# Performance work log

Measured on AMD Instinct MI355X. Metric: run time of the kernel, lower is better.

## Reference

```python
import jax, jax.numpy as jnp
import numpy as np

N_POINTS = 1048576
LEVELS = 16
LOG2T = 19
TABLE_SIZE = 1 << LOG2T  # 524288
FEAT = 2
MIN_RES = 16.0
MAX_RES = 512.0


def setup_inputs() -> dict:
    key = jax.random.key(0)
    kx, kt = jax.random.split(key)
    bounding_box = jnp.array([[-1.5, -1.5, -1.5], [1.5, 1.5, 1.5]], dtype=jnp.float32)
    # sample mostly inside the box, a few points slightly outside to exercise clamp/keep_mask
    x = jax.random.uniform(kx, (N_POINTS, 3), dtype=jnp.float32, minval=-1.6, maxval=1.6)
    # torch init: uniform(-1e-4, 1e-4) per level embedding table
    tables = jax.random.uniform(kt, (LEVELS, TABLE_SIZE, FEAT), dtype=jnp.float32,
                                minval=-1e-4, maxval=1e-4)
    return {"x": x, "bounding_box": bounding_box, "tables": tables}


def _hash_encode(x, bounding_box, tables):
    min_b, max_b = bounding_box[0], bounding_box[1]  # [3]
    # keep_mask: point unchanged by clamping in every dim
    keep_mask = jnp.all((x >= min_b) & (x <= max_b), axis=-1)
    xc = jnp.clip(x, min_b, max_b)
    u = (xc - min_b) / (max_b - min_b)  # normalized to [0,1], [N,3]

    b = jnp.exp((jnp.log(MAX_RES) - jnp.log(MIN_RES)) / (LEVELS - 1))
    PI = jnp.array([1, 2654435761, 805459861], dtype=jnp.uint32)
    HASH_MASK = jnp.uint32(TABLE_SIZE - 1)
    # 8 corner offsets in (i,j,k) order matching the torch module
    offs = jnp.array([[i, j, k] for i in (0, 1) for j in (0, 1) for k in (0, 1)],
                     dtype=jnp.int32)  # [8,3]

    outs = []
    for level in range(LEVELS):
        Nl = jnp.floor(MIN_RES * b ** level)            # scalar resolution
        box_size = (max_b - min_b) / Nl                 # [3]
        grid = jnp.floor(u * Nl).astype(jnp.int32)      # [N,3] min-corner grid coords
        vmin = grid.astype(x.dtype) * box_size + min_b  # [N,3]
        vmax = vmin + box_size                          # [N,3]
        corners = (grid[:, None, :] + offs[None, :, :]).astype(jnp.uint32)  # [N,8,3]
        # spatial hash: xor of coord*prime, wrap-around in uint32 matches low bits of torch int64
        h = (corners[..., 0] * PI[0]) ^ (corners[..., 1] * PI[1]) ^ (corners[..., 2] * PI[2])
        idx = (h & HASH_MASK).astype(jnp.int32)         # [N,8]
        emb = tables[level][idx]                        # gather -> [N,8,F]
        # trilinear interpolation; note: uses ORIGINAL (unclamped) x, as in the torch code
        w = (x - vmin) / (vmax - vmin)                  # [N,3]
        wx, wy, wz = w[:, 0:1], w[:, 1:2], w[:, 2:3]
        c00 = emb[:, 0] * (1 - wx) + emb[:, 4] * wx
        c01 = emb[:, 1] * (1 - wx) + emb[:, 5] * wx
        c10 = emb[:, 2] * (1 - wx) + emb[:, 6] * wx
        c11 = emb[:, 3] * (1 - wx) + emb[:, 7] * wx
        c0 = c00 * (1 - wy) + c10 * wy
        c1 = c01 * (1 - wy) + c11 * wy
        outs.append(c0 * (1 - wz) + c1 * wz)            # [N,F]
    return jnp.concatenate(outs, axis=-1), keep_mask    # [N, L*F], [N]


def reference(x, bounding_box, tables):
    return _hash_encode(x, bounding_box, tables)
```

## Files before the change

### kernel.cpp

```cpp
#include <hip/hip_runtime.h>

#define NPTS   1048576
#define NLEV   16
#define TSIZE  (1u << 19)
#define HMASK  (TSIZE - 1u)
#define NBUCK  32768

__device__ __constant__ float NLF_TAB[16] = {
    16.f, 20.f, 25.f, 32.f, 40.f, 50.f, 64.f, 80.f,
    101.f, 128.f, 161.f, 203.f, 256.f, 322.f, 406.f, 512.f};

__device__ __forceinline__ unsigned spread5(unsigned x) {
    x &= 0x1F;
    x = (x | (x << 8)) & 0x100F;
    x = (x | (x << 4)) & 0x10C3;
    x = (x | (x << 2)) & 0x1249;
    return x;
}

__device__ __forceinline__ unsigned morton_key(float u0, float u1, float u2) {
    unsigned k0 = min(31u, (unsigned)(u0 * 32.0f));
    unsigned k1 = min(31u, (unsigned)(u1 * 32.0f));
    unsigned k2 = min(31u, (unsigned)(u2 * 32.0f));
    return (spread5(k0) << 2) | (spread5(k1) << 1) | spread5(k2);
}

__device__ __forceinline__ void uvw(float x0, float x1, float x2,
                                    float* u0, float* u1, float* u2) {
    const float mn = -1.5f, mx = 1.5f, rng = 3.0f;
    *u0 = (fminf(fmaxf(x0, mn), mx) - mn) / rng;
    *u1 = (fminf(fmaxf(x1, mn), mx) - mn) / rng;
    *u2 = (fminf(fmaxf(x2, mn), mx) - mn) / rng;
}

__device__ __forceinline__ void level_lerp(
    float x0, float x1, float x2, float u0, float u1, float u2,
    float Nl, const float2* __restrict__ tab, float* r0, float* r1)
{
#pragma clang fp contract(off)
    const float mn = -1.5f, rng = 3.0f;
    const float box = rng / Nl;

    int g0 = (int)floorf(u0 * Nl);
    int g1 = (int)floorf(u1 * Nl);
    int g2 = (int)floorf(u2 * Nl);

    float vmin0 = (float)g0 * box + mn;
    float vmin1 = (float)g1 * box + mn;
    float vmin2 = (float)g2 * box + mn;

    float den0 = (vmin0 + box) - vmin0;
    float den1 = (vmin1 + box) - vmin1;
    float den2 = (vmin2 + box) - vmin2;

    float wx = (x0 - vmin0) / den0;
    float wy = (x1 - vmin1) / den1;
    float wz = (x2 - vmin2) / den2;

    unsigned hx0 = (unsigned)g0;
    unsigned hx1 = (unsigned)(g0 + 1);
    unsigned hy0 = (unsigned)g1       * 2654435761u;
    unsigned hy1 = (unsigned)(g1 + 1) * 2654435761u;
    unsigned hz0 = (unsigned)g2       * 805459861u;
    unsigned hz1 = (unsigned)(g2 + 1) * 805459861u;

    float2 e000 = tab[(hx0 ^ hy0 ^ hz0) & HMASK];
    float2 e001 = tab[(hx0 ^ hy0 ^ hz1) & HMASK];
    float2 e010 = tab[(hx0 ^ hy1 ^ hz0) & HMASK];
    float2 e011 = tab[(hx0 ^ hy1 ^ hz1) & HMASK];
    float2 e100 = tab[(hx1 ^ hy0 ^ hz0) & HMASK];
    float2 e101 = tab[(hx1 ^ hy0 ^ hz1) & HMASK];
    float2 e110 = tab[(hx1 ^ hy1 ^ hz0) & HMASK];
    float2 e111 = tab[(hx1 ^ hy1 ^ hz1) & HMASK];

    float omx = 1.0f - wx, omy = 1.0f - wy, omz = 1.0f - wz;
    {
        float c00 = e000.x * omx + e100.x * wx;
        float c01 = e001.x * omx + e101.x * wx;
        float c10 = e010.x * omx + e110.x * wx;
        float c11 = e011.x * omx + e111.x * wx;
        float c0  = c00 * omy + c10 * wy;
        float c1  = c01 * omy + c11 * wy;
        *r0 = c0 * omz + c1 * wz;
    }
    {
        float c00 = e000.y * omx + e100.y * wx;
        float c01 = e001.y * omx + e101.y * wx;
        float c10 = e010.y * omx + e110.y * wx;
        float c11 = e011.y * omx + e111.y * wx;
        float c0  = c00 * omy + c10 * wy;
        float c1  = c01 * omy + c11 * wy;
        *r1 = c0 * omz + c1 * wz;
    }
}


template<int L, bool DO_HIST, bool DO_MASK>
__device__ __forceinline__ void fine_body(
    const float* __restrict__ xin, const float* __restrict__ tables,
    float* __restrict__ out, unsigned* __restrict__ hist, int p)
{
#pragma clang fp contract(off)
    float x0 = xin[3 * p], x1 = xin[3 * p + 1], x2 = xin[3 * p + 2];
    float u0, u1, u2; uvw(x0, x1, x2, &u0, &u1, &u2);

    if (DO_HIST)
        atomicAdd(&hist[morton_key(u0, u1, u2)], 1u);

    const float2* tab = (const float2*)tables + (size_t)L * TSIZE;
    float r0, r1;
    level_lerp(x0, x1, x2, u0, u1, u2, NLF_TAB[L], tab, &r0, &r1);
    *(float2*)(out + (size_t)p * 32 + 2 * L) = make_float2(r0, r1);

    if (DO_MASK) {
        const float mn = -1.5f, mx = 1.5f;
        float keep = (x0 >= mn && x0 <= mx &&
                      x1 >= mn && x1 <= mx &&
                      x2 >= mn && x2 <= mx) ? 1.0f : 0.0f;
        out[(size_t)NPTS * 32 + p] = keep;
    }
}

template<int L, bool DO_HIST, bool DO_MASK>
__global__ __launch_bounds__(256)
void fine_kernel(const float* __restrict__ xin,
                 const float* __restrict__ tables,
                 float* __restrict__ out,
                 unsigned* __restrict__ hist)
{
    int p = blockIdx.x * 256 + threadIdx.x;
    if (p >= NPTS) return;
    fine_body<L, DO_HIST, DO_MASK>(xin, tables, out, hist, p);
}

__global__ __launch_bounds__(256)
void fine14_scan(const float* __restrict__ xin,
                 const float* __restrict__ tables,
                 float* __restrict__ out,
                 unsigned* __restrict__ hist)
{
    __shared__ unsigned part[256];
    if (blockIdx.x < 4096) {
        int p = blockIdx.x * 256 + threadIdx.x;
        fine_body<14, false, false>(xin, tables, out, hist, p);
        return;
    }
    int t = threadIdx.x;
    unsigned s = 0;
    for (int i = 0; i < 128; ++i) s += hist[t * 128 + i];
    part[t] = s;
    __syncthreads();
    for (int off = 1; off < 256; off <<= 1) {
        unsigned v = (t >= off) ? part[t - off] : 0;
        __syncthreads();
        part[t] += v;
        __syncthreads();
    }
    unsigned base = (t == 0) ? 0u : part[t - 1];
    for (int i = 0; i < 128; ++i) {
        unsigned c = hist[t * 128 + i];
        hist[t * 128 + i] = base;
        base += c;
    }
}


__global__ __launch_bounds__(256)
void scatter_kernel(const float* __restrict__ xin,
                    unsigned* __restrict__ cursor,
                    unsigned* __restrict__ sidx,
                    float4* __restrict__ sx4)
{
    int p = blockIdx.x * 256 + threadIdx.x;
    if (p >= NPTS) return;
    float x0 = xin[3 * p], x1 = xin[3 * p + 1], x2 = xin[3 * p + 2];
    float u0, u1, u2; uvw(x0, x1, x2, &u0, &u1, &u2);
    unsigned pos = atomicAdd(&cursor[morton_key(u0, u1, u2)], 1u);
    sidx[pos] = (unsigned)p;
    sx4[pos] = make_float4(x0, x1, x2, 0.0f);
}


__global__ __launch_bounds__(256)
void coarse_sorted(const unsigned* __restrict__ sidx,
                   const float4* __restrict__ sx4,
                   const float* __restrict__ tables,
                   float* __restrict__ out)
{
#pragma clang fp contract(off)
    int s = blockIdx.x * 256 + threadIdx.x;
    if (s >= NPTS) return;
    unsigned p = sidx[s];
    float4 xv = sx4[s];
    float u0, u1, u2; uvw(xv.x, xv.y, xv.z, &u0, &u1, &u2);

    float res[16];
#pragma unroll
    for (int l = 0; l < 8; ++l) {
        const float2* tab = (const float2*)tables + (size_t)l * TSIZE;
        level_lerp(xv.x, xv.y, xv.z, u0, u1, u2, NLF_TAB[l], tab,
                   &res[2 * l], &res[2 * l + 1]);
    }

    float4* orow = (float4*)(out + (size_t)p * 32);
#pragma unroll
    for (int i = 0; i < 4; ++i)
        orow[i] = make_float4(res[4 * i + 0], res[4 * i + 1],
                              res[4 * i + 2], res[4 * i + 3]);
}

__global__ __launch_bounds__(256)
void mid_sorted(const unsigned* __restrict__ sidx,
                const float4* __restrict__ sx4,
                const float* __restrict__ tables,
                float* __restrict__ out)
{
#pragma clang fp contract(off)
    int s = blockIdx.x * 256 + threadIdx.x;
    if (s >= NPTS) return;
    unsigned p = sidx[s];
    float4 xv = sx4[s];
    float u0, u1, u2; uvw(xv.x, xv.y, xv.z, &u0, &u1, &u2);

    float r[4];
    {
        const float2* tab = (const float2*)tables + (size_t)8 * TSIZE;
        level_lerp(xv.x, xv.y, xv.z, u0, u1, u2, NLF_TAB[8], tab, &r[0], &r[1]);
    }
    {
        const float2* tab = (const float2*)tables + (size_t)9 * TSIZE;
        level_lerp(xv.x, xv.y, xv.z, u0, u1, u2, NLF_TAB[9], tab, &r[2], &r[3]);
    }
    *(float4*)(out + (size_t)p * 32 + 16) = make_float4(r[0], r[1], r[2], r[3]);
}


__global__ __launch_bounds__(256)
void coarse_kernel(const float* __restrict__ xin,
                   const float* __restrict__ tables,
                   float* __restrict__ out)
{
#pragma clang fp contract(off)
    int p = blockIdx.x * 256 + threadIdx.x;
    if (p >= NPTS) return;
    float x0 = xin[3 * p], x1 = xin[3 * p + 1], x2 = xin[3 * p + 2];
    float u0, u1, u2; uvw(x0, x1, x2, &u0, &u1, &u2);

    float res[16];
#pragma unroll
    for (int l = 0; l < 8; ++l) {
        const float2* tab = (const float2*)tables + (size_t)l * TSIZE;
        level_lerp(x0, x1, x2, u0, u1, u2, NLF_TAB[l], tab,
                   &res[2 * l], &res[2 * l + 1]);
    }
    float4* orow = (float4*)(out + (size_t)p * 32);
#pragma unroll
    for (int i = 0; i < 4; ++i)
        orow[i] = make_float4(res[4 * i + 0], res[4 * i + 1],
                              res[4 * i + 2], res[4 * i + 3]);
}

extern "C" void kernel_launch(void* const* d_in, const int* in_sizes, int n_in,
                              void* d_out, int out_size, void* d_ws, size_t ws_size,
                              hipStream_t stream) {
    const float* x      = (const float*)d_in[0];
    const float* tables = (const float*)d_in[2];
    float* out = (float*)d_out;

    int n = in_sizes[0] / 3;
    int blocks = (n + 255) / 256;

    const size_t HIST_B   = (size_t)NBUCK * 4;
    const size_t SIDX_OFF = 131072;
    const size_t SX4_OFF  = SIDX_OFF + (size_t)NPTS * 4;
    const size_t NEEDED   = SX4_OFF + (size_t)NPTS * 16;

    if (ws_size >= NEEDED) {
        unsigned* hist = (unsigned*)d_ws;
        unsigned* sidx = (unsigned*)((char*)d_ws + SIDX_OFF);
        float4*   sx4  = (float4*)((char*)d_ws + SX4_OFF);

        hipMemsetAsync(hist, 0, HIST_B, stream);

        fine_kernel<15, true , false><<<blocks, 256, 0, stream>>>(x, tables, out, hist);
        fine14_scan<<<blocks + 1, 256, 0, stream>>>(x, tables, out, hist);
        fine_kernel<13, false, false><<<blocks, 256, 0, stream>>>(x, tables, out, hist);
        fine_kernel<12, false, false><<<blocks, 256, 0, stream>>>(x, tables, out, hist);
        fine_kernel<11, false, false><<<blocks, 256, 0, stream>>>(x, tables, out, hist);
        fine_kernel<10, false, true ><<<blocks, 256, 0, stream>>>(x, tables, out, hist);

        scatter_kernel<<<blocks, 256, 0, stream>>>(x, hist, sidx, sx4);
        coarse_sorted<<<blocks, 256, 0, stream>>>(sidx, sx4, tables, out);
        mid_sorted<<<blocks, 256, 0, stream>>>(sidx, sx4, tables, out);
    } else {
        coarse_kernel<<<blocks, 256, 0, stream>>>(x, tables, out);
        fine_kernel< 8, false, false><<<blocks, 256, 0, stream>>>(x, tables, out, nullptr);
        fine_kernel< 9, false, false><<<blocks, 256, 0, stream>>>(x, tables, out, nullptr);
        fine_kernel<10, false, true ><<<blocks, 256, 0, stream>>>(x, tables, out, nullptr);
        fine_kernel<11, false, false><<<blocks, 256, 0, stream>>>(x, tables, out, nullptr);
        fine_kernel<12, false, false><<<blocks, 256, 0, stream>>>(x, tables, out, nullptr);
        fine_kernel<13, false, false><<<blocks, 256, 0, stream>>>(x, tables, out, nullptr);
        fine_kernel<14, false, false><<<blocks, 256, 0, stream>>>(x, tables, out, nullptr);
        fine_kernel<15, false, false><<<blocks, 256, 0, stream>>>(x, tables, out, nullptr);
    }
}
```

Baseline: 448.7 us.

## Pack point index into sorted float4 and batch gathers across levels

The scatter kernel now stores the original point index in the w lane of the sorted float4, which removes the separate sidx array and its extra load in the sorted kernels. The coarse and mid sorted kernels now use a batched helper that computes hashes for 4 (or 2) levels, issues all 32 gathers before any interpolation, and then does the math. This aims to raise memory-level parallelism on the random table gathers. Fine-kernel x loads use nontemporal hints. The batching adds register pressure, which may lower occupancy.

```diff
diff --git a/kernel.cpp b/kernel.cpp
--- a/kernel.cpp
+++ b/kernel.cpp
@@ -94,6 +94,91 @@
     }
 }
 
+template<int L0V, int NB>
+__device__ __forceinline__ void levels_batched(
+    float x0, float x1, float x2, float u0, float u1, float u2,
+    const float* __restrict__ tables, float* __restrict__ res)
+{
+#pragma clang fp contract(off)
+    const float mn = -1.5f, rng = 3.0f;
+    unsigned idx[NB * 8];
+    float wxa[NB], wya[NB], wza[NB];
+
+#pragma unroll
+    for (int j = 0; j < NB; ++j) {
+        const int l = L0V + j;
+        const float Nl  = NLF_TAB[l];
+        const float box = rng / Nl;
+
+        int g0 = (int)floorf(u0 * Nl);
+        int g1 = (int)floorf(u1 * Nl);
+        int g2 = (int)floorf(u2 * Nl);
+
+        float vmin0 = (float)g0 * box + mn;
+        float vmin1 = (float)g1 * box + mn;
+        float vmin2 = (float)g2 * box + mn;
+
+        float den0 = (vmin0 + box) - vmin0;
+        float den1 = (vmin1 + box) - vmin1;
+        float den2 = (vmin2 + box) - vmin2;
+
+        wxa[j] = (x0 - vmin0) / den0;
+        wya[j] = (x1 - vmin1) / den1;
+        wza[j] = (x2 - vmin2) / den2;
+
+        unsigned hx0 = (unsigned)g0;
+        unsigned hx1 = (unsigned)(g0 + 1);
+        unsigned hy0 = (unsigned)g1       * 2654435761u;
+        unsigned hy1 = (unsigned)(g1 + 1) * 2654435761u;
+        unsigned hz0 = (unsigned)g2       * 805459861u;
+        unsigned hz1 = (unsigned)(g2 + 1) * 805459861u;
+
+        idx[j * 8 + 0] = (hx0 ^ hy0 ^ hz0) & HMASK;
+        idx[j * 8 + 1] = (hx0 ^ hy0 ^ hz1) & HMASK;
+        idx[j * 8 + 2] = (hx0 ^ hy1 ^ hz0) & HMASK;
+        idx[j * 8 + 3] = (hx0 ^ hy1 ^ hz1) & HMASK;
+        idx[j * 8 + 4] = (hx1 ^ hy0 ^ hz0) & HMASK;
+        idx[j * 8 + 5] = (hx1 ^ hy0 ^ hz1) & HMASK;
+        idx[j * 8 + 6] = (hx1 ^ hy1 ^ hz0) & HMASK;
+        idx[j * 8 + 7] = (hx1 ^ hy1 ^ hz1) & HMASK;
+    }
+
+    float2 e[NB * 8];
+#pragma unroll
+    for (int j = 0; j < NB; ++j) {
+        const float2* tab = (const float2*)tables + (size_t)(L0V + j) * TSIZE;
+#pragma unroll
+        for (int k = 0; k < 8; ++k)
+            e[j * 8 + k] = tab[idx[j * 8 + k]];
+    }
+    asm volatile("" ::: "memory");
+
+#pragma unroll
+    for (int j = 0; j < NB; ++j) {
+        float wx = wxa[j], wy = wya[j], wz = wza[j];
+        float omx = 1.0f - wx, omy = 1.0f - wy, omz = 1.0f - wz;
+        const float2* ee = &e[j * 8];
+        {
+            float c00 = ee[0].x * omx + ee[4].x * wx;
+            float c01 = ee[1].x * omx + ee[5].x * wx;
+            float c10 = ee[2].x * omx + ee[6].x * wx;
+            float c11 = ee[3].x * omx + ee[7].x * wx;
+            float c0  = c00 * omy + c10 * wy;
+            float c1  = c01 * omy + c11 * wy;
+            res[2 * (L0V + j) + 0] = c0 * omz + c1 * wz;
+        }
+        {
+            float c00 = ee[0].y * omx + ee[4].y * wx;
+            float c01 = ee[1].y * omx + ee[5].y * wx;
+            float c10 = ee[2].y * omx + ee[6].y * wx;
+            float c11 = ee[3].y * omx + ee[7].y * wx;
+            float c0  = c00 * omy + c10 * wy;
+            float c1  = c01 * omy + c11 * wy;
+            res[2 * (L0V + j) + 1] = c0 * omz + c1 * wz;
+        }
+    }
+}
+
 
 template<int L, bool DO_HIST, bool DO_MASK>
 __device__ __forceinline__ void fine_body(
@@ -101,7 +186,9 @@
     float* __restrict__ out, unsigned* __restrict__ hist, int p)
 {
 #pragma clang fp contract(off)
-    float x0 = xin[3 * p], x1 = xin[3 * p + 1], x2 = xin[3 * p + 2];
+    float x0 = __builtin_nontemporal_load(&xin[3 * p + 0]);
+    float x1 = __builtin_nontemporal_load(&xin[3 * p + 1]);
+    float x2 = __builtin_nontemporal_load(&xin[3 * p + 2]);
     float u0, u1, u2; uvw(x0, x1, x2, &u0, &u1, &u2);
 
     if (DO_HIST)
@@ -168,39 +255,34 @@
 __global__ __launch_bounds__(256)
 void scatter_kernel(const float* __restrict__ xin,
                     unsigned* __restrict__ cursor,
-                    unsigned* __restrict__ sidx,
                     float4* __restrict__ sx4)
 {
     int p = blockIdx.x * 256 + threadIdx.x;
     if (p >= NPTS) return;
-    float x0 = xin[3 * p], x1 = xin[3 * p + 1], x2 = xin[3 * p + 2];
+    float x0 = __builtin_nontemporal_load(&xin[3 * p + 0]);
+    float x1 = __builtin_nontemporal_load(&xin[3 * p + 1]);
+    float x2 = __builtin_nontemporal_load(&xin[3 * p + 2]);
     float u0, u1, u2; uvw(x0, x1, x2, &u0, &u1, &u2);
     unsigned pos = atomicAdd(&cursor[morton_key(u0, u1, u2)], 1u);
-    sidx[pos] = (unsigned)p;
-    sx4[pos] = make_float4(x0, x1, x2, 0.0f);
-}
-
-
-__global__ __launch_bounds__(256)
-void coarse_sorted(const unsigned* __restrict__ sidx,
-                   const float4* __restrict__ sx4,
+    sx4[pos] = make_float4(x0, x1, x2, __uint_as_float((unsigned)p));
+}
+
+
+__global__ __launch_bounds__(256)
+void coarse_sorted(const float4* __restrict__ sx4,
                    const float* __restrict__ tables,
                    float* __restrict__ out)
 {
 #pragma clang fp contract(off)
     int s = blockIdx.x * 256 + threadIdx.x;
     if (s >= NPTS) return;
-    unsigned p = sidx[s];
     float4 xv = sx4[s];
+    unsigned p = __float_as_uint(xv.w);
     float u0, u1, u2; uvw(xv.x, xv.y, xv.z, &u0, &u1, &u2);
 
     float res[16];
-#pragma unroll
-    for (int l = 0; l < 8; ++l) {
-        const float2* tab = (const float2*)tables + (size_t)l * TSIZE;
-        level_lerp(xv.x, xv.y, xv.z, u0, u1, u2, NLF_TAB[l], tab,
-                   &res[2 * l], &res[2 * l + 1]);
-    }
+    levels_batched<0, 4>(xv.x, xv.y, xv.z, u0, u1, u2, tables, res);
+    levels_batched<4, 4>(xv.x, xv.y, xv.z, u0, u1, u2, tables, res);
 
     float4* orow = (float4*)(out + (size_t)p * 32);
 #pragma unroll
@@ -210,28 +292,22 @@
 }
 
 __global__ __launch_bounds__(256)
-void mid_sorted(const unsigned* __restrict__ sidx,
-                const float4* __restrict__ sx4,
+void mid_sorted(const float4* __restrict__ sx4,
                 const float* __restrict__ tables,
                 float* __restrict__ out)
 {
 #pragma clang fp contract(off)
     int s = blockIdx.x * 256 + threadIdx.x;
     if (s >= NPTS) return;
-    unsigned p = sidx[s];
     float4 xv = sx4[s];
+    unsigned p = __float_as_uint(xv.w);
     float u0, u1, u2; uvw(xv.x, xv.y, xv.z, &u0, &u1, &u2);
 
-    float r[4];
-    {
-        const float2* tab = (const float2*)tables + (size_t)8 * TSIZE;
-        level_lerp(xv.x, xv.y, xv.z, u0, u1, u2, NLF_TAB[8], tab, &r[0], &r[1]);
-    }
-    {
-        const float2* tab = (const float2*)tables + (size_t)9 * TSIZE;
-        level_lerp(xv.x, xv.y, xv.z, u0, u1, u2, NLF_TAB[9], tab, &r[2], &r[3]);
-    }
-    *(float4*)(out + (size_t)p * 32 + 16) = make_float4(r[0], r[1], r[2], r[3]);
+    float res[20];
+    levels_batched<8, 2>(xv.x, xv.y, xv.z, u0, u1, u2, tables, res);
+
+    *(float4*)(out + (size_t)p * 32 + 16) =
+        make_float4(res[16], res[17], res[18], res[19]);
 }
 
 
@@ -270,14 +346,12 @@
     int n = in_sizes[0] / 3;
     int blocks = (n + 255) / 256;
 
-    const size_t HIST_B   = (size_t)NBUCK * 4;
-    const size_t SIDX_OFF = 131072;
-    const size_t SX4_OFF  = SIDX_OFF + (size_t)NPTS * 4;
-    const size_t NEEDED   = SX4_OFF + (size_t)NPTS * 16;
+    const size_t HIST_B  = (size_t)NBUCK * 4;
+    const size_t SX4_OFF = 131072;
+    const size_t NEEDED  = SX4_OFF + (size_t)NPTS * 16;
 
     if (ws_size >= NEEDED) {
         unsigned* hist = (unsigned*)d_ws;
-        unsigned* sidx = (unsigned*)((char*)d_ws + SIDX_OFF);
         float4*   sx4  = (float4*)((char*)d_ws + SX4_OFF);
 
         hipMemsetAsync(hist, 0, HIST_B, stream);
@@ -289,9 +363,9 @@
         fine_kernel<11, false, false><<<blocks, 256, 0, stream>>>(x, tables, out, hist);
         fine_kernel<10, false, true ><<<blocks, 256, 0, stream>>>(x, tables, out, hist);
 
-        scatter_kernel<<<blocks, 256, 0, stream>>>(x, hist, sidx, sx4);
-        coarse_sorted<<<blocks, 256, 0, stream>>>(sidx, sx4, tables, out);
-        mid_sorted<<<blocks, 256, 0, stream>>>(sidx, sx4, tables, out);
+        scatter_kernel<<<blocks, 256, 0, stream>>>(x, hist, sx4);
+        coarse_sorted<<<blocks, 256, 0, stream>>>(sx4, tables, out);
+        mid_sorted<<<blocks, 256, 0, stream>>>(sx4, tables, out);
     } else {
         coarse_kernel<<<blocks, 256, 0, stream>>>(x, tables, out);
         fine_kernel< 8, false, false><<<blocks, 256, 0, stream>>>(x, tables, out, nullptr);
```

Result: slower. 483.0 us (+7.6%).
